# Kernel optimization log

Hardware: AMD Instinct MI355X
Metric: run time of the kernel (lower is better)

Reference implementation:

```python
import jax, jax.numpy as jnp
import numpy as np

LN_EPS = 1e-5

def setup_inputs() -> dict:
    key = jax.random.key(0)
    ks = jax.random.split(key, 5)
    B, S, Dv, Dl, V = 4, 576, 1024, 4096, 32000
    return {
        "vision_feats": jax.random.normal(ks[0], (B, S, Dv), dtype=jnp.float32),
        "W1_w": jax.random.normal(ks[1], (Dl, Dv), dtype=jnp.float32) * (Dv ** -0.5),
        "W1_b": jax.random.normal(ks[2], (Dl,), dtype=jnp.float32) * 0.02,
        "W2_w": jax.random.normal(ks[3], (V, Dl), dtype=jnp.float32) * (Dl ** -0.5),
        "llm_token_embed": jax.random.normal(ks[4], (V, Dl), dtype=jnp.float32) * 0.02,
    }

def reference(vision_feats, W1_w, W1_b, W2_w, llm_token_embed):
    # W1: (B,S,Dv) @ (Dv,Dl) + b -> (B,S,Dl)
    x = jnp.einsum('bsd,ed->bse', vision_feats, W1_w) + W1_b
    # layer_norm over last dim, no affine params
    mu = jnp.mean(x, axis=-1, keepdims=True)
    var = jnp.mean(jnp.square(x - mu), axis=-1, keepdims=True)
    xn = (x - mu) * jax.lax.rsqrt(var + LN_EPS)
    # W2 (no bias): (B,S,Dl) -> (B,S,V) vocab logits
    logits = jnp.einsum('bse,ve->bsv', xn, W2_w)
    P = jax.nn.softmax(logits, axis=-1)
    # softmax-weighted mixture of LLM token embeddings: (B,S,V) @ (V,Dl)
    F_align = jnp.einsum('bsv,ve->bse', P, llm_token_embed)
    return F_align
```

## Files before the change

kernel.cpp:

```cpp
#include <hip/hip_runtime.h>
#include <hip/hip_bf16.h>
#include <stdint.h>

typedef __bf16 bf16_t;
typedef __attribute__((ext_vector_type(8))) __bf16 bf16x8;
typedef __attribute__((ext_vector_type(4))) __bf16 bf16x4;
typedef __attribute__((ext_vector_type(4))) float f32x4;
typedef __attribute__((ext_vector_type(8))) unsigned short u16x8;

#define M_TOK 2304
#define DV    1024
#define DLAT  4096
#define VOCAB 32000

__device__ __forceinline__ float bf2f(unsigned short u) {
  union { unsigned int i; float f; } v; v.i = ((unsigned int)u) << 16; return v.f;
}
__device__ __forceinline__ bf16_t f2bf(float f) { return (bf16_t)f; }

#define GLOAD16(gp, lp) \
  __builtin_amdgcn_global_load_lds( \
      (const __attribute__((address_space(1))) unsigned int*)(const void*)(gp), \
      (__attribute__((address_space(3))) unsigned int*)(void*)(lp), 16, 0, 0)

constexpr int GBM = 96, GBN = 128, GBK = 32;

template<int EPI>
__global__ void __launch_bounds__(256, 4)
gemm_bb(const bf16_t* __restrict__ Ap, const bf16_t* __restrict__ Bp,
        void* __restrict__ Cp, int K, int ldc, int Mt)
{
  __shared__ __align__(16) bf16_t Al[2][GBM * GBK];
  __shared__ __align__(16) bf16_t Bl[2][GBN * GBK];

  const int nwg = gridDim.x;
  const int orig = blockIdx.x;
  const int q = nwg >> 3, r = nwg & 7;
  const int xcd = orig & 7, idx = orig >> 3;
  const int wg = (xcd < r ? xcd * (q + 1) : r * (q + 1) + (xcd - r) * q) + idx;
  const int mt = wg % Mt, nt = wg / Mt;
  const int m0 = mt * GBM, n0 = nt * GBN;

  const int t    = threadIdx.x;
  const int lane = t & 63, wv = t >> 6;
  const int wm = wv >> 1, wn = wv & 1;
  const int lr = lane & 15, kc = lane >> 4;

  f32x4 acc[3][4];
#pragma unroll
  for (int i = 0; i < 3; ++i)
#pragma unroll
    for (int j = 0; j < 4; ++j)
#pragma unroll
      for (int x = 0; x < 4; ++x) acc[i][j][x] = 0.0f;

  const int rql = lane >> 2;
  const int cb  = (lane & 3) * 16;
  const size_t rstride = (size_t)K * 2;

  const int NT = K / GBK;

  auto STAGE = [&](int kt, int nb) {
    const size_t kb = (size_t)kt * GBK * 2;
    if (wv < 3) {
      const char* g1 = (const char*)Ap + (size_t)(m0 + wv * 32 + rql) * rstride + kb + cb;
      char* l1 = (char*)&Al[nb][0] + wv * 2048;
      GLOAD16(g1, l1);
      GLOAD16(g1 + 16 * rstride, l1 + 1024);
    }
    {
      const char* g1 = (const char*)Bp + (size_t)(n0 + wv * 32 + rql) * rstride + kb + cb;
      char* l1 = (char*)&Bl[nb][0] + wv * 2048;
      GLOAD16(g1, l1);
      GLOAD16(g1 + 16 * rstride, l1 + 1024);
    }
  };

  auto COMPUTE = [&](int nb) {
    bf16x8 af[3], bfv[4];
#pragma unroll
    for (int f = 0; f < 3; ++f)
      af[f] = *(const bf16x8*)(&Al[nb][(wm * 48 + f * 16 + lr) * GBK + kc * 8]);
#pragma unroll
    for (int f = 0; f < 4; ++f)
      bfv[f] = *(const bf16x8*)(&Bl[nb][(wn * 64 + f * 16 + lr) * GBK + kc * 8]);
    __builtin_amdgcn_s_setprio(1);
#pragma unroll
    for (int i = 0; i < 3; ++i)
#pragma unroll
      for (int j = 0; j < 4; ++j)
        acc[i][j] = __builtin_amdgcn_mfma_f32_16x16x32_bf16(af[i], bfv[j], acc[i][j], 0, 0, 0);
    __builtin_amdgcn_s_setprio(0);
  };

  STAGE(0, 0);
  __syncthreads();
  int cur = 0;
  for (int kt = 0; kt < NT; ++kt) {
    const bool more = (kt + 1) < NT;
    if (more) STAGE(kt + 1, cur ^ 1);
    COMPUTE(cur);
    __syncthreads();
    cur ^= 1;
  }

#pragma unroll
  for (int j = 0; j < 4; ++j) {
    const int col = n0 + wn * 64 + j * 16 + lr;
#pragma unroll
    for (int i = 0; i < 3; ++i) {
      const int row = m0 + wm * 48 + i * 16 + kc * 4;
      f32x4 a4 = acc[i][j];
      if (EPI == 1) {
        bf16_t* C = (bf16_t*)Cp;
#pragma unroll
        for (int x = 0; x < 4; ++x) C[(size_t)(row + x) * ldc + col] = f2bf(a4[x]);
      } else {
        float* C = (float*)Cp;
#pragma unroll
        for (int x = 0; x < 4; ++x) C[(size_t)(row + x) * ldc + col] = a4[x];
      }
    }
  }
}

constexpr int BM = 128, BN = 128, BK = 32;
constexpr int SA = 40;

__device__ __forceinline__ void bar_lds() {
  asm volatile("s_waitcnt lgkmcnt(0)" ::: "memory");
  __builtin_amdgcn_s_barrier();
}

template<int AMODE, int BMODE, int EPI>
__global__ void __launch_bounds__(256, 2)
gemm_k(const void* __restrict__ Ap, const float* __restrict__ Bp,
       void* __restrict__ Cp, const float* __restrict__ bias,
       int K, int lda, int ldb, int ldc, int Mt)
{
  __shared__ __align__(16) bf16_t Al[2][BM * SA];
  __shared__ __align__(16) bf16_t Bl[2][BN * SA];

  const int nwg = gridDim.x;
  const int orig = blockIdx.x;
  const int q = nwg >> 3, r = nwg & 7;
  const int xcd = orig & 7, idx = orig >> 3;
  const int wg = (xcd < r ? xcd * (q + 1) : r * (q + 1) + (xcd - r) * q) + idx;
  const int mt = wg % Mt, nt = wg / Mt;
  const int m0 = mt * BM, n0 = nt * BN;

  const int t    = threadIdx.x;
  const int lane = t & 63, wv = t >> 6;
  const int wm = wv >> 1, wn = wv & 1;
  const int lr = lane & 15, kc = lane >> 4;

  f32x4 acc[4][4];
#pragma unroll
  for (int i = 0; i < 4; ++i)
#pragma unroll
    for (int j = 0; j < 4; ++j)
#pragma unroll
      for (int x = 0; x < 4; ++x) acc[i][j][x] = 0.0f;

  const int sr = t >> 1, sh = t & 1;
  const int tv = t & 7, te = t >> 3;

  bf16x8 s1_ab0, s1_ab1;          bf16x8 s2_ab0, s2_ab1;
  f32x4  s1_af0, s1_af1, s1_af2, s1_af3;
  f32x4  s2_af0, s2_af1, s2_af2, s2_af3;
  f32x4  s1_b0, s1_b1, s1_b2, s1_b3;
  f32x4  s2_b0, s2_b1, s2_b2, s2_b3;

  const int NT = K / BK;

  auto LOADS1 = [&](int kt) {
    const int k0 = kt * BK;
    if (AMODE == 0) {
      const bf16_t* asrc = (const bf16_t*)Ap + (size_t)(m0 + sr) * lda + k0 + sh * 16;
      s1_ab0 = *(const bf16x8*)(asrc);
      s1_ab1 = *(const bf16x8*)(asrc + 8);
    } else {
      const float* asrc = (const float*)Ap + (size_t)(m0 + sr) * lda + k0 + sh * 16;
      s1_af0 = *(const f32x4*)(asrc);     s1_af1 = *(const f32x4*)(asrc + 4);
      s1_af2 = *(const f32x4*)(asrc + 8); s1_af3 = *(const f32x4*)(asrc + 12);
    }
    if (BMODE == 0) {
      const float* bsrc = Bp + (size_t)(n0 + sr) * ldb + k0 + sh * 16;
      s1_b0 = *(const f32x4*)(bsrc);     s1_b1 = *(const f32x4*)(bsrc + 4);
      s1_b2 = *(const f32x4*)(bsrc + 8); s1_b3 = *(const f32x4*)(bsrc + 12);
    } else {
      const float* bsrc = Bp + (size_t)(k0 + tv * 4) * ldb + n0 + te * 4;
      s1_b0 = *(const f32x4*)(bsrc);
      s1_b1 = *(const f32x4*)(bsrc + (size_t)ldb);
      s1_b2 = *(const f32x4*)(bsrc + (size_t)2 * ldb);
      s1_b3 = *(const f32x4*)(bsrc + (size_t)3 * ldb);
    }
  };
  auto LOADS2 = [&](int kt) {
    const int k0 = kt * BK;
    if (AMODE == 0) {
      const bf16_t* asrc = (const bf16_t*)Ap + (size_t)(m0 + sr) * lda + k0 + sh * 16;
      s2_ab0 = *(const bf16x8*)(asrc);
      s2_ab1 = *(const bf16x8*)(asrc + 8);
    } else {
      const float* asrc = (const float*)Ap + (size_t)(m0 + sr) * lda + k0 + sh * 16;
      s2_af0 = *(const f32x4*)(asrc);     s2_af1 = *(const f32x4*)(asrc + 4);
      s2_af2 = *(const f32x4*)(asrc + 8); s2_af3 = *(const f32x4*)(asrc + 12);
    }
    if (BMODE == 0) {
      const float* bsrc = Bp + (size_t)(n0 + sr) * ldb + k0 + sh * 16;
      s2_b0 = *(const f32x4*)(bsrc);     s2_b1 = *(const f32x4*)(bsrc + 4);
      s2_b2 = *(const f32x4*)(bsrc + 8); s2_b3 = *(const f32x4*)(bsrc + 12);
    } else {
      const float* bsrc = Bp + (size_t)(k0 + tv * 4) * ldb + n0 + te * 4;
      s2_b0 = *(const f32x4*)(bsrc);
      s2_b1 = *(const f32x4*)(bsrc + (size_t)ldb);
      s2_b2 = *(const f32x4*)(bsrc + (size_t)2 * ldb);
      s2_b3 = *(const f32x4*)(bsrc + (size_t)3 * ldb);
    }
  };

  auto STORE1 = [&](int nb) {
    {
      bf16x8 w0, w1;
      if (AMODE == 0) { w0 = s1_ab0; w1 = s1_ab1; }
      else {
#pragma unroll
        for (int c = 0; c < 4; ++c) {
          w0[c] = f2bf(s1_af0[c]); w0[c + 4] = f2bf(s1_af1[c]);
          w1[c] = f2bf(s1_af2[c]); w1[c + 4] = f2bf(s1_af3[c]);
        }
      }
      bf16_t* dst = &Al[nb][sr * SA + sh * 16];
      *(bf16x8*)(dst) = w0; *(bf16x8*)(dst + 8) = w1;
    }
    if (BMODE == 0) {
      bf16x8 w0, w1;
#pragma unroll
      for (int c = 0; c < 4; ++c) {
        w0[c] = f2bf(s1_b0[c]); w0[c + 4] = f2bf(s1_b1[c]);
        w1[c] = f2bf(s1_b2[c]); w1[c + 4] = f2bf(s1_b3[c]);
      }
      bf16_t* dst = &Bl[nb][sr * SA + sh * 16];
      *(bf16x8*)(dst) = w0; *(bf16x8*)(dst + 8) = w1;
    } else {
#pragma unroll
      for (int i = 0; i < 4; ++i) {
        bf16x4 w4;
        w4[0] = f2bf(s1_b0[i]); w4[1] = f2bf(s1_b1[i]);
        w4[2] = f2bf(s1_b2[i]); w4[3] = f2bf(s1_b3[i]);
        *(bf16x4*)(&Bl[nb][(te * 4 + i) * SA + tv * 4]) = w4;
      }
    }
  };
  auto STORE2 = [&](int nb) {
    {
      bf16x8 w0, w1;
      if (AMODE == 0) { w0 = s2_ab0; w1 = s2_ab1; }
      else {
#pragma unroll
        for (int c = 0; c < 4; ++c) {
          w0[c] = f2bf(s2_af0[c]); w0[c + 4] = f2bf(s2_af1[c]);
          w1[c] = f2bf(s2_af2[c]); w1[c + 4] = f2bf(s2_af3[c]);
        }
      }
      bf16_t* dst = &Al[nb][sr * SA + sh * 16];
      *(bf16x8*)(dst) = w0; *(bf16x8*)(dst + 8) = w1;
    }
    if (BMODE == 0) {
      bf16x8 w0, w1;
#pragma unroll
      for (int c = 0; c < 4; ++c) {
        w0[c] = f2bf(s2_b0[c]); w0[c + 4] = f2bf(s2_b1[c]);
        w1[c] = f2bf(s2_b2[c]); w1[c + 4] = f2bf(s2_b3[c]);
      }
      bf16_t* dst = &Bl[nb][sr * SA + sh * 16];
      *(bf16x8*)(dst) = w0; *(bf16x8*)(dst + 8) = w1;
    } else {
#pragma unroll
      for (int i = 0; i < 4; ++i) {
        bf16x4 w4;
        w4[0] = f2bf(s2_b0[i]); w4[1] = f2bf(s2_b1[i]);
        w4[2] = f2bf(s2_b2[i]); w4[3] = f2bf(s2_b3[i]);
        *(bf16x4*)(&Bl[nb][(te * 4 + i) * SA + tv * 4]) = w4;
      }
    }
  };

  auto COMPUTE = [&](int nb) {
    bf16x8 af[4], bfv[4];
#pragma unroll
    for (int f = 0; f < 4; ++f)
      af[f] = *(const bf16x8*)(&Al[nb][(wm * 64 + f * 16 + lr) * SA + kc * 8]);
#pragma unroll
    for (int f = 0; f < 4; ++f)
      bfv[f] = *(const bf16x8*)(&Bl[nb][(wn * 64 + f * 16 + lr) * SA + kc * 8]);
    __builtin_amdgcn_s_setprio(1);
#pragma unroll
    for (int i = 0; i < 4; ++i)
#pragma unroll
      for (int j = 0; j < 4; ++j)
        acc[i][j] = __builtin_amdgcn_mfma_f32_16x16x32_bf16(af[i], bfv[j], acc[i][j], 0, 0, 0);
    __builtin_amdgcn_s_setprio(0);
  };

  LOADS1(0);
  LOADS2(1);
  STORE1(0);
  bar_lds();

  const int NIT = NT / 2 - 1;
  for (int it = 0; it < NIT; ++it) {
    LOADS1(2 * it + 2);
    COMPUTE(0);
    STORE2(1);
    bar_lds();
    LOADS2(2 * it + 3);
    COMPUTE(1);
    STORE1(0);
    bar_lds();
  }
  COMPUTE(0);
  STORE2(1);
  bar_lds();
  COMPUTE(1);

#pragma unroll
  for (int j = 0; j < 4; ++j) {
    const int col = n0 + wn * 64 + j * 16 + lr;
    float bv = 0.0f;
    if (EPI == 0) bv = bias[col];
#pragma unroll
    for (int i = 0; i < 4; ++i) {
      const int row = m0 + wm * 64 + i * 16 + kc * 4;
      f32x4 a4 = acc[i][j];
      if (EPI == 0) {
        float* C = (float*)Cp;
#pragma unroll
        for (int x = 0; x < 4; ++x) C[(size_t)(row + x) * ldc + col] = a4[x] + bv;
      } else if (EPI == 1) {
        bf16_t* C = (bf16_t*)Cp;
#pragma unroll
        for (int x = 0; x < 4; ++x) C[(size_t)(row + x) * ldc + col] = f2bf(a4[x]);
      } else {
        float* C = (float*)Cp;
#pragma unroll
        for (int x = 0; x < 4; ++x) C[(size_t)(row + x) * ldc + col] = a4[x];
      }
    }
  }
}

__global__ void __launch_bounds__(256)
cvt_bf16_k(const float* __restrict__ in, bf16_t* __restrict__ out, long n8)
{
  const long stride = (long)gridDim.x * 256;
  for (long i = (long)blockIdx.x * 256 + threadIdx.x; i < n8; i += stride) {
    f32x4 a = *(const f32x4*)(in + i * 8);
    f32x4 b = *(const f32x4*)(in + i * 8 + 4);
    bf16x8 o;
#pragma unroll
    for (int j = 0; j < 4; ++j) { o[j] = f2bf(a[j]); o[j + 4] = f2bf(b[j]); }
    *(bf16x8*)(out + i * 8) = o;
  }
}

__global__ void __launch_bounds__(256)
embT_k(const float* __restrict__ E, bf16_t* __restrict__ ET)
{
  __shared__ bf16_t tl[64][72];
  const int vb = blockIdx.x % (VOCAB / 64);
  const int eb = blockIdx.x / (VOCAB / 64);
  const int v0 = vb * 64, e0 = eb * 64;
  const int t = threadIdx.x;

  const int rr = t >> 4, c4 = (t & 15) * 4;
#pragma unroll
  for (int p = 0; p < 4; ++p) {
    const float* src = E + (size_t)(v0 + rr + p * 16) * DLAT + e0 + c4;
    f32x4 a = *(const f32x4*)src;
#pragma unroll
    for (int j = 0; j < 4; ++j) tl[c4 + j][rr + p * 16] = f2bf(a[j]);
  }
  __syncthreads();

  const int el = t >> 3, v8 = (t & 7) * 8;
#pragma unroll
  for (int p = 0; p < 2; ++p) {
    bf16x8 o = *(const bf16x8*)(&tl[el + p * 32][v8]);
    *(bf16x8*)(ET + (size_t)(e0 + el + p * 32) * VOCAB + v0 + v8) = o;
  }
}

__global__ void __launch_bounds__(256)
ln_k(const float* __restrict__ x, bf16_t* __restrict__ xn)
{
  __shared__ float sm[4];
  const int row = blockIdx.x, t = threadIdx.x;
  const float* xr = x + (size_t)row * DLAT;
  f32x4 v[4];
#pragma unroll
  for (int i = 0; i < 4; ++i) v[i] = *(const f32x4*)(xr + (t + i * 256) * 4);

  float s = 0.0f;
#pragma unroll
  for (int i = 0; i < 4; ++i)
#pragma unroll
    for (int j = 0; j < 4; ++j) s += v[i][j];
#pragma unroll
  for (int o = 32; o > 0; o >>= 1) s += __shfl_xor(s, o, 64);
  if ((t & 63) == 0) sm[t >> 6] = s;
  __syncthreads();
  const float mean = (sm[0] + sm[1] + sm[2] + sm[3]) * (1.0f / DLAT);
  __syncthreads();

  float qv = 0.0f;
#pragma unroll
  for (int i = 0; i < 4; ++i)
#pragma unroll
    for (int j = 0; j < 4; ++j) { float d = v[i][j] - mean; qv += d * d; }
#pragma unroll
  for (int o = 32; o > 0; o >>= 1) qv += __shfl_xor(qv, o, 64);
  if ((t & 63) == 0) sm[t >> 6] = qv;
  __syncthreads();
  const float varr = (sm[0] + sm[1] + sm[2] + sm[3]) * (1.0f / DLAT);
  const float rs = rsqrtf(varr + 1e-5f);

  bf16_t* outr = xn + (size_t)row * DLAT;
#pragma unroll
  for (int i = 0; i < 4; ++i) {
    bf16x4 o;
#pragma unroll
    for (int j = 0; j < 4; ++j) o[j] = f2bf((v[i][j] - mean) * rs);
    *(bf16x4*)(outr + (t + i * 256) * 4) = o;
  }
}

__global__ void __launch_bounds__(256)
softmax_k(bf16_t* __restrict__ L)
{
  __shared__ __align__(16) bf16_t rs_[VOCAB];
  __shared__ float sm[4];
  const int row = blockIdx.x, t = threadIdx.x;
  bf16_t* lrow = L + (size_t)row * VOCAB;
  const int NF = VOCAB / 8;

  float m = -3.0e38f;
  for (int f = t; f < NF; f += 256) {
    u16x8 u = *(const u16x8*)(&lrow[f * 8]);
    *(u16x8*)(&rs_[f * 8]) = u;
#pragma unroll
    for (int j = 0; j < 8; ++j) m = fmaxf(m, bf2f(u[j]));
  }
#pragma unroll
  for (int o = 32; o > 0; o >>= 1) m = fmaxf(m, __shfl_xor(m, o, 64));
  if ((t & 63) == 0) sm[t >> 6] = m;
  __syncthreads();
  m = fmaxf(fmaxf(sm[0], sm[1]), fmaxf(sm[2], sm[3]));
  __syncthreads();

  float s = 0.0f;
  for (int f = t; f < NF; f += 256) {
    u16x8 u = *(const u16x8*)(&rs_[f * 8]);
#pragma unroll
    for (int j = 0; j < 8; ++j) s += __expf(bf2f(u[j]) - m);
  }
#pragma unroll
  for (int o = 32; o > 0; o >>= 1) s += __shfl_xor(s, o, 64);
  if ((t & 63) == 0) sm[t >> 6] = s;
  __syncthreads();
  const float inv = 1.0f / (sm[0] + sm[1] + sm[2] + sm[3]);

  for (int f = t; f < NF; f += 256) {
    u16x8 u = *(const u16x8*)(&rs_[f * 8]);
    bf16x8 o;
#pragma unroll
    for (int j = 0; j < 8; ++j) o[j] = f2bf(__expf(bf2f(u[j]) - m) * inv);
    *(bf16x8*)(&lrow[f * 8]) = o;
  }
}

extern "C" void kernel_launch(void* const* d_in, const int* in_sizes, int n_in,
                              void* d_out, int out_size, void* d_ws, size_t ws_size,
                              hipStream_t stream)
{
  (void)in_sizes; (void)n_in; (void)out_size;
  const float* vision = (const float*)d_in[0];
  const float* W1w    = (const float*)d_in[1];
  const float* W1b    = (const float*)d_in[2];
  const float* W2w    = (const float*)d_in[3];
  const float* Emb    = (const float*)d_in[4];
  float* out = (float*)d_out;

  char* ws = (char*)d_ws;
  bf16_t* xn     = (bf16_t*)ws;
  bf16_t* logits = (bf16_t*)(ws + 18874368);
  float*  xbuf   = (float*)(ws + 18874368 + 147456000);
  bf16_t* wslot  = (bf16_t*)(ws + 18874368 + 147456000 + 37748736);

  const size_t NEED = 18874368ull + 147456000ull + 37748736ull + 262144000ull;

  gemm_k<1, 0, 0><<<dim3((M_TOK / BM) * (DLAT / BN)), dim3(256), 0, stream>>>(
      vision, W1w, xbuf, W1b, DV, DV, DV, DLAT, M_TOK / BM);

  ln_k<<<dim3(M_TOK), dim3(256), 0, stream>>>(xbuf, xn);

  if (ws_size >= NEED) {
    cvt_bf16_k<<<dim3(2048), dim3(256), 0, stream>>>(W2w, wslot, (long)VOCAB * DLAT / 8);
    gemm_bb<1><<<dim3((M_TOK / GBM) * (VOCAB / GBN)), dim3(256), 0, stream>>>(
        xn, wslot, logits, DLAT, VOCAB, M_TOK / GBM);
    embT_k<<<dim3((VOCAB / 64) * (DLAT / 64)), dim3(256), 0, stream>>>(Emb, wslot);
    softmax_k<<<dim3(M_TOK), dim3(256), 0, stream>>>(logits);
    gemm_bb<2><<<dim3((M_TOK / GBM) * (DLAT / GBN)), dim3(256), 0, stream>>>(
        logits, wslot, out, VOCAB, DLAT, M_TOK / GBM);
  } else {
    gemm_k<0, 0, 1><<<dim3((M_TOK / BM) * (VOCAB / BN)), dim3(256), 0, stream>>>(
        xn, W2w, logits, nullptr, DLAT, DLAT, DLAT, VOCAB, M_TOK / BM);
    softmax_k<<<dim3(M_TOK), dim3(256), 0, stream>>>(logits);
    gemm_k<0, 1, 2><<<dim3((M_TOK / BM) * (DLAT / BN)), dim3(256), 0, stream>>>(
        logits, Emb, out, nullptr, VOCAB, VOCAB, DLAT, DLAT, M_TOK / BM);
  }
}
```

Before: 2.135 ms.

## Use triple-buffered 128x128 bf16 GEMM for all three matmuls

```diff
diff --git a/kernel.cpp b/kernel.cpp
--- a/kernel.cpp
+++ b/kernel.cpp
@@ -23,15 +23,16 @@
       (const __attribute__((address_space(1))) unsigned int*)(const void*)(gp), \
       (__attribute__((address_space(3))) unsigned int*)(void*)(lp), 16, 0, 0)
 
-constexpr int GBM = 96, GBN = 128, GBK = 32;
+constexpr int GBM = 128, GBN = 128, GBK = 32;
 
 template<int EPI>
-__global__ void __launch_bounds__(256, 4)
+__global__ void __launch_bounds__(256, 3)
 gemm_bb(const bf16_t* __restrict__ Ap, const bf16_t* __restrict__ Bp,
-        void* __restrict__ Cp, int K, int ldc, int Mt)
-{
-  __shared__ __align__(16) bf16_t Al[2][GBM * GBK];
-  __shared__ __align__(16) bf16_t Bl[2][GBN * GBK];
+        void* __restrict__ Cp, const float* __restrict__ bias,
+        int K, int ldc, int Mt)
+{
+  __shared__ __align__(16) bf16_t Al[3][GBM * GBK];
+  __shared__ __align__(16) bf16_t Bl[3][GBN * GBK];
 
   const int nwg = gridDim.x;
   const int orig = blockIdx.x;
@@ -46,9 +47,9 @@
   const int wm = wv >> 1, wn = wv & 1;
   const int lr = lane & 15, kc = lane >> 4;
 
-  f32x4 acc[3][4];
-#pragma unroll
-  for (int i = 0; i < 3; ++i)
+  f32x4 acc[4][4];
+#pragma unroll
+  for (int i = 0; i < 4; ++i)
 #pragma unroll
     for (int j = 0; j < 4; ++j)
 #pragma unroll
@@ -62,54 +63,64 @@
 
   auto STAGE = [&](int kt, int nb) {
     const size_t kb = (size_t)kt * GBK * 2;
-    if (wv < 3) {
-      const char* g1 = (const char*)Ap + (size_t)(m0 + wv * 32 + rql) * rstride + kb + cb;
-      char* l1 = (char*)&Al[nb][0] + wv * 2048;
-      GLOAD16(g1, l1);
-      GLOAD16(g1 + 16 * rstride, l1 + 1024);
-    }
-    {
-      const char* g1 = (const char*)Bp + (size_t)(n0 + wv * 32 + rql) * rstride + kb + cb;
-      char* l1 = (char*)&Bl[nb][0] + wv * 2048;
-      GLOAD16(g1, l1);
-      GLOAD16(g1 + 16 * rstride, l1 + 1024);
-    }
+    const char* ga = (const char*)Ap + (size_t)(m0 + wv * 32 + rql) * rstride + kb + cb;
+    char* la = (char*)&Al[nb][0] + wv * 2048;
+    GLOAD16(ga, la);
+    GLOAD16(ga + 16 * rstride, la + 1024);
+    const char* gb = (const char*)Bp + (size_t)(n0 + wv * 32 + rql) * rstride + kb + cb;
+    char* lb = (char*)&Bl[nb][0] + wv * 2048;
+    GLOAD16(gb, lb);
+    GLOAD16(gb + 16 * rstride, lb + 1024);
   };
 
   auto COMPUTE = [&](int nb) {
-    bf16x8 af[3], bfv[4];
-#pragma unroll
-    for (int f = 0; f < 3; ++f)
-      af[f] = *(const bf16x8*)(&Al[nb][(wm * 48 + f * 16 + lr) * GBK + kc * 8]);
+    bf16x8 af[4], bfv[4];
+#pragma unroll
+    for (int f = 0; f < 4; ++f)
+      af[f] = *(const bf16x8*)(&Al[nb][(wm * 64 + f * 16 + lr) * GBK + kc * 8]);
 #pragma unroll
     for (int f = 0; f < 4; ++f)
       bfv[f] = *(const bf16x8*)(&Bl[nb][(wn * 64 + f * 16 + lr) * GBK + kc * 8]);
     __builtin_amdgcn_s_setprio(1);
 #pragma unroll
-    for (int i = 0; i < 3; ++i)
+    for (int i = 0; i < 4; ++i)
 #pragma unroll
       for (int j = 0; j < 4; ++j)
         acc[i][j] = __builtin_amdgcn_mfma_f32_16x16x32_bf16(af[i], bfv[j], acc[i][j], 0, 0, 0);
     __builtin_amdgcn_s_setprio(0);
   };
 
+  auto BARX = [&]() {
+    asm volatile("s_waitcnt lgkmcnt(0)" ::: "memory");
+    __builtin_amdgcn_s_barrier();
+  };
+
   STAGE(0, 0);
-  __syncthreads();
-  int cur = 0;
-  for (int kt = 0; kt < NT; ++kt) {
-    const bool more = (kt + 1) < NT;
-    if (more) STAGE(kt + 1, cur ^ 1);
-    COMPUTE(cur);
-    __syncthreads();
-    cur ^= 1;
-  }
+  STAGE(1, 1);
+  asm volatile("s_waitcnt vmcnt(4)" ::: "memory");
+  __builtin_amdgcn_s_barrier();
+
+  int bc = 0, bn = 1, bs = 2;
+  for (int kt = 0; kt < NT - 2; ++kt) {
+    STAGE(kt + 2, bs);
+    COMPUTE(bc);
+    asm volatile("s_waitcnt vmcnt(4)" ::: "memory");
+    BARX();
+    const int tmp = bc; bc = bn; bn = bs; bs = tmp;
+  }
+  COMPUTE(bc);
+  asm volatile("s_waitcnt vmcnt(0)" ::: "memory");
+  BARX();
+  COMPUTE(bn);
 
 #pragma unroll
   for (int j = 0; j < 4; ++j) {
     const int col = n0 + wn * 64 + j * 16 + lr;
-#pragma unroll
-    for (int i = 0; i < 3; ++i) {
-      const int row = m0 + wm * 48 + i * 16 + kc * 4;
+    float bv = 0.0f;
+    if (EPI == 0) bv = bias[col];
+#pragma unroll
+    for (int i = 0; i < 4; ++i) {
+      const int row = m0 + wm * 64 + i * 16 + kc * 4;
       f32x4 a4 = acc[i][j];
       if (EPI == 1) {
         bf16_t* C = (bf16_t*)Cp;
@@ -118,7 +129,7 @@
       } else {
         float* C = (float*)Cp;
 #pragma unroll
-        for (int x = 0; x < 4; ++x) C[(size_t)(row + x) * ldc + col] = a4[x];
+        for (int x = 0; x < 4; ++x) C[(size_t)(row + x) * ldc + col] = a4[x] + bv;
       }
     }
   }
@@ -495,25 +506,31 @@
   char* ws = (char*)d_ws;
   bf16_t* xn     = (bf16_t*)ws;
   bf16_t* logits = (bf16_t*)(ws + 18874368);
-  float*  xbuf   = (float*)(ws + 18874368 + 147456000);
-  bf16_t* wslot  = (bf16_t*)(ws + 18874368 + 147456000 + 37748736);
-
-  const size_t NEED = 18874368ull + 147456000ull + 37748736ull + 262144000ull;
-
-  gemm_k<1, 0, 0><<<dim3((M_TOK / BM) * (DLAT / BN)), dim3(256), 0, stream>>>(
-      vision, W1w, xbuf, W1b, DV, DV, DV, DLAT, M_TOK / BM);
-
-  ln_k<<<dim3(M_TOK), dim3(256), 0, stream>>>(xbuf, xn);
+  float*  xbuf   = (float*)(ws + 166330368);
+  bf16_t* wslot  = (bf16_t*)(ws + 204079104);
+  bf16_t* xnv    = (bf16_t*)(ws + 466223104);
+  bf16_t* w1b    = (bf16_t*)(ws + 470941696);
+  const size_t NEED = 479330304ull;
+
+  const int Mt = M_TOK / GBM;
 
   if (ws_size >= NEED) {
+    cvt_bf16_k<<<dim3(512), dim3(256), 0, stream>>>(vision, xnv, (long)M_TOK * DV / 8);
+    cvt_bf16_k<<<dim3(512), dim3(256), 0, stream>>>(W1w, w1b, (long)DLAT * DV / 8);
+    gemm_bb<0><<<dim3(Mt * (DLAT / GBN)), dim3(256), 0, stream>>>(
+        xnv, w1b, xbuf, W1b, DV, DLAT, Mt);
+    ln_k<<<dim3(M_TOK), dim3(256), 0, stream>>>(xbuf, xn);
     cvt_bf16_k<<<dim3(2048), dim3(256), 0, stream>>>(W2w, wslot, (long)VOCAB * DLAT / 8);
-    gemm_bb<1><<<dim3((M_TOK / GBM) * (VOCAB / GBN)), dim3(256), 0, stream>>>(
-        xn, wslot, logits, DLAT, VOCAB, M_TOK / GBM);
+    gemm_bb<1><<<dim3(Mt * (VOCAB / GBN)), dim3(256), 0, stream>>>(
+        xn, wslot, logits, nullptr, DLAT, VOCAB, Mt);
     embT_k<<<dim3((VOCAB / 64) * (DLAT / 64)), dim3(256), 0, stream>>>(Emb, wslot);
     softmax_k<<<dim3(M_TOK), dim3(256), 0, stream>>>(logits);
-    gemm_bb<2><<<dim3((M_TOK / GBM) * (DLAT / GBN)), dim3(256), 0, stream>>>(
-        logits, wslot, out, VOCAB, DLAT, M_TOK / GBM);
+    gemm_bb<2><<<dim3(Mt * (DLAT / GBN)), dim3(256), 0, stream>>>(
+        logits, wslot, out, nullptr, VOCAB, DLAT, Mt);
   } else {
+    gemm_k<1, 0, 0><<<dim3((M_TOK / BM) * (DLAT / BN)), dim3(256), 0, stream>>>(
+        vision, W1w, xbuf, W1b, DV, DV, DV, DLAT, M_TOK / BM);
+    ln_k<<<dim3(M_TOK), dim3(256), 0, stream>>>(xbuf, xn);
     gemm_k<0, 0, 1><<<dim3((M_TOK / BM) * (VOCAB / BN)), dim3(256), 0, stream>>>(
         xn, W2w, logits, nullptr, DLAT, DLAT, DLAT, VOCAB, M_TOK / BM);
     softmax_k<<<dim3(M_TOK), dim3(256), 0, stream>>>(logits);
```

Result: faster. 1.978 ms (-7.4%).
